# Optimization experiments

Measured on AMD Instinct MI355X. Metric: run time of the kernel, lower is better.

## Reference

```python
import jax, jax.numpy as jnp
import numpy as np

B, D, C, K = 131072, 512, 5, 10  # batch, emb_dim, num_classes, k experts


def setup_inputs() -> dict:
    key = jax.random.key(0)
    k1, k2, k3, k4, k5 = jax.random.split(key, 5)
    s = 1.0 / np.sqrt(D)
    return {
        "emb": jax.random.normal(k1, (B, D), dtype=jnp.float32),
        "We": jax.random.normal(k2, (K, D, C), dtype=jnp.float32) * s,
        "be": jax.random.normal(k3, (K, C), dtype=jnp.float32) * s,
        "Wg": jax.random.normal(k4, (D, K), dtype=jnp.float32) * s,
        "bg": jax.random.normal(k5, (K,), dtype=jnp.float32) * s,
    }


def reference(emb, We, be, Wg, bg):
    # gate: softmax over experts, [B, K]
    g = jax.nn.softmax(emb @ Wg + bg, axis=1)
    # all experts as one batched GEMM: [B, K, C], then ReLU
    e = jax.nn.relu(jnp.einsum('bd,kdc->bkc', emb, We) + be[None, :, :])
    # gate-weighted sum over experts -> [B, C]
    return jnp.einsum('bkc,bk->bc', e, g)
```

## Files before the change

### kernel.cpp

```cpp
#include <hip/hip_runtime.h>
#include <hip/hip_bf16.h>
#include <math.h>

#define BATCH   131072
#define DIM     512
#define NCLS    5
#define NEXP    10
#define NW      60
#define NCOL    64
#define PACK_TPB 256
#define TPB     512
#define ROWS_PER_BLOCK 128
#define EPS_STRIDE 68

typedef short bf16x8 __attribute__((ext_vector_type(8)));
typedef float f32x4  __attribute__((ext_vector_type(4)));

__global__ void pack_w_kernel(const float* __restrict__ We,
                              const float* __restrict__ be,
                              const float* __restrict__ Wg,
                              const float* __restrict__ bg,
                              unsigned short* __restrict__ wfrag,
                              float* __restrict__ bpack) {
    int idx = blockIdx.x * PACK_TPB + threadIdx.x;
    int c    = idx >> 11;
    int t    = (idx >> 9) & 3;
    int lane = (idx >> 3) & 63;
    int j    = idx & 7;
    int d = c * 32 + (lane >> 4) * 8 + j;
    int n = t * 16 + (lane & 15);
    float v = 0.0f;
    if (n < NEXP) {
        v = Wg[d * NEXP + n];
    } else if (n < NW) {
        int k  = (n - NEXP) / NCLS;
        int cc = (n - NEXP) % NCLS;
        v = We[(k * DIM + d) * NCLS + cc];
    }
    wfrag[idx] = __builtin_bit_cast(unsigned short, __float2bfloat16(v));
    if (idx < NCOL) {
        float bv = 0.0f;
        if (idx < NEXP) bv = bg[idx];
        else if (idx < NW) {
            int k  = (idx - NEXP) / NCLS;
            int cc = (idx - NEXP) % NCLS;
            bv = be[k * NCLS + cc];
        }
        bpack[idx] = bv;
    }
}

__global__ __launch_bounds__(TPB) void moe_mfma_kernel(
        const float* __restrict__ emb,
        const float4* __restrict__ wfrag4,
        const float* __restrict__ bpack,
        float* __restrict__ out) {
    __shared__ float4 smem4[4096];

    const int tid = threadIdx.x;

    #pragma unroll
    for (int i = 0; i < 8; ++i)
        smem4[i * TPB + tid] = wfrag4[i * TPB + tid];
    __syncthreads();

    const int w = tid >> 6;
    const int L = tid & 63;
    const int r = L & 15;
    const int q = L >> 4;

    const size_t rowBase = (size_t)blockIdx.x * ROWS_PER_BLOCK + w * 16;
    const float* arow = emb + (rowBase + r) * DIM + q * 8;
    const bf16x8* bl = reinterpret_cast<const bf16x8*>(smem4);

    f32x4 acc0 = {0.f, 0.f, 0.f, 0.f};
    f32x4 acc1 = acc0, acc2 = acc0, acc3 = acc0;

    #pragma unroll 4
    for (int c = 0; c < DIM / 32; ++c) {
        const float4* a4 = reinterpret_cast<const float4*>(arow + (size_t)c * 32);
        float4 a0 = a4[0];
        float4 a1 = a4[1];
        bf16x8 b0 = bl[(c * 4 + 0) * 64 + L];
        bf16x8 b1 = bl[(c * 4 + 1) * 64 + L];
        bf16x8 b2 = bl[(c * 4 + 2) * 64 + L];
        bf16x8 b3 = bl[(c * 4 + 3) * 64 + L];
        float av[8] = {a0.x, a0.y, a0.z, a0.w, a1.x, a1.y, a1.z, a1.w};
        bf16x8 af;
        #pragma unroll
        for (int j = 0; j < 8; ++j)
            af[j] = (short)__builtin_bit_cast(unsigned short, __float2bfloat16(av[j]));
        acc0 = __builtin_amdgcn_mfma_f32_16x16x32_bf16(af, b0, acc0, 0, 0, 0);
        acc1 = __builtin_amdgcn_mfma_f32_16x16x32_bf16(af, b1, acc1, 0, 0, 0);
        acc2 = __builtin_amdgcn_mfma_f32_16x16x32_bf16(af, b2, acc2, 0, 0, 0);
        acc3 = __builtin_amdgcn_mfma_f32_16x16x32_bf16(af, b3, acc3, 0, 0, 0);
    }

    __syncthreads();
    float* eps = reinterpret_cast<float*>(smem4);
    #pragma unroll
    for (int i = 0; i < 4; ++i) {
        int rowl = w * 16 + q * 4 + i;
        eps[rowl * EPS_STRIDE +  0 + r] = acc0[i];
        eps[rowl * EPS_STRIDE + 16 + r] = acc1[i];
        eps[rowl * EPS_STRIDE + 32 + r] = acc2[i];
        eps[rowl * EPS_STRIDE + 48 + r] = acc3[i];
    }
    __syncthreads();

    if (tid < ROWS_PER_BLOCK) {
        const float* row = eps + tid * EPS_STRIDE;
        float g[NEXP];
        float m = -INFINITY;
        #pragma unroll
        for (int k = 0; k < NEXP; ++k) {
            g[k] = row[k] + bpack[k];
            m = fmaxf(m, g[k]);
        }
        float s = 0.0f;
        #pragma unroll
        for (int k = 0; k < NEXP; ++k) {
            g[k] = __expf(g[k] - m);
            s += g[k];
        }
        float inv = 1.0f / s;

        float o[NCLS] = {0.f, 0.f, 0.f, 0.f, 0.f};
        #pragma unroll
        for (int k = 0; k < NEXP; ++k) {
            float gk = g[k] * inv;
            #pragma unroll
            for (int cc = 0; cc < NCLS; ++cc) {
                int n = NEXP + k * NCLS + cc;
                float e = row[n] + bpack[n];
                e = fmaxf(e, 0.0f);
                o[cc] = fmaf(gk, e, o[cc]);
            }
        }
        size_t ob = ((size_t)blockIdx.x * ROWS_PER_BLOCK + tid) * NCLS;
        #pragma unroll
        for (int cc = 0; cc < NCLS; ++cc) out[ob + cc] = o[cc];
    }
}

extern "C" void kernel_launch(void* const* d_in, const int* in_sizes, int n_in,
                              void* d_out, int out_size, void* d_ws, size_t ws_size,
                              hipStream_t stream) {
    const float* emb = (const float*)d_in[0];
    const float* We  = (const float*)d_in[1];
    const float* be  = (const float*)d_in[2];
    const float* Wg  = (const float*)d_in[3];
    const float* bg  = (const float*)d_in[4];
    float* out = (float*)d_out;

    unsigned short* wfrag = (unsigned short*)d_ws;
    float* bpack = (float*)((char*)d_ws + 32768 * sizeof(unsigned short));

    pack_w_kernel<<<(16 * 4 * 64 * 8) / PACK_TPB, PACK_TPB, 0, stream>>>(
        We, be, Wg, bg, wfrag, bpack);
    moe_mfma_kernel<<<BATCH / ROWS_PER_BLOCK, TPB, 0, stream>>>(
        emb, (const float4*)wfrag, bpack, out);
}
```

Before: 362.3 us.

## Process two 16-row tiles per wave with software-prefetched A loads

Each wave now computes 32 rows, so every B fragment read from LDS feeds two MFMAs, and the block covers 256 rows. The next k-step's emb loads are issued before the current step's MFMAs to hide global latency. The epilogue stride shrinks to 61 and skips unused columns so 256 rows fit in LDS. In exchange, register pressure rises with eight accumulators and prefetch buffers, and the grid has half as many blocks.

```diff
diff --git a/kernel.cpp b/kernel.cpp
--- a/kernel.cpp
+++ b/kernel.cpp
@@ -10,8 +10,8 @@
 #define NCOL    64
 #define PACK_TPB 256
 #define TPB     512
-#define ROWS_PER_BLOCK 128
-#define EPS_STRIDE 68
+#define ROWS_PER_BLOCK 256
+#define EPS_STRIDE 61
 
 typedef short bf16x8 __attribute__((ext_vector_type(8)));
 typedef float f32x4  __attribute__((ext_vector_type(4)));
@@ -50,7 +50,34 @@
     }
 }
 
-__global__ __launch_bounds__(TPB) void moe_mfma_kernel(
+#define CVT8(DST, VA, VB) do {                                               \
+    float _v[8] = {(VA).x, (VA).y, (VA).z, (VA).w,                           \
+                   (VB).x, (VB).y, (VB).z, (VB).w};                          \
+    _Pragma("unroll")                                                        \
+    for (int _j = 0; _j < 8; ++_j)                                           \
+        (DST)[_j] = (short)__builtin_bit_cast(unsigned short,                \
+                         __float2bfloat16(_v[_j]));                          \
+} while (0)
+
+#define KSTEP(C, A0A, A0B, A1A, A1B) do {                                    \
+    bf16x8 _b0 = bl[((C) * 4 + 0) * 64 + L];                                 \
+    bf16x8 _b1 = bl[((C) * 4 + 1) * 64 + L];                                 \
+    bf16x8 _b2 = bl[((C) * 4 + 2) * 64 + L];                                 \
+    bf16x8 _b3 = bl[((C) * 4 + 3) * 64 + L];                                 \
+    bf16x8 _af0, _af1;                                                       \
+    CVT8(_af0, A0A, A0B);                                                    \
+    CVT8(_af1, A1A, A1B);                                                    \
+    acc0[0] = __builtin_amdgcn_mfma_f32_16x16x32_bf16(_af0, _b0, acc0[0], 0, 0, 0); \
+    acc1[0] = __builtin_amdgcn_mfma_f32_16x16x32_bf16(_af1, _b0, acc1[0], 0, 0, 0); \
+    acc0[1] = __builtin_amdgcn_mfma_f32_16x16x32_bf16(_af0, _b1, acc0[1], 0, 0, 0); \
+    acc1[1] = __builtin_amdgcn_mfma_f32_16x16x32_bf16(_af1, _b1, acc1[1], 0, 0, 0); \
+    acc0[2] = __builtin_amdgcn_mfma_f32_16x16x32_bf16(_af0, _b2, acc0[2], 0, 0, 0); \
+    acc1[2] = __builtin_amdgcn_mfma_f32_16x16x32_bf16(_af1, _b2, acc1[2], 0, 0, 0); \
+    acc0[3] = __builtin_amdgcn_mfma_f32_16x16x32_bf16(_af0, _b3, acc0[3], 0, 0, 0); \
+    acc1[3] = __builtin_amdgcn_mfma_f32_16x16x32_bf16(_af1, _b3, acc1[3], 0, 0, 0); \
+} while (0)
+
+__global__ __launch_bounds__(TPB, 4) void moe_mfma_kernel(
         const float* __restrict__ emb,
         const float4* __restrict__ wfrag4,
         const float* __restrict__ bpack,
@@ -58,53 +85,63 @@
     __shared__ float4 smem4[4096];
 
     const int tid = threadIdx.x;
+    const int w = tid >> 6;
+    const int L = tid & 63;
+    const int r = L & 15;
+    const int q = L >> 4;
+
+    const size_t rowBase = (size_t)blockIdx.x * ROWS_PER_BLOCK + w * 32;
+    const float* ap0 = emb + (rowBase + r) * DIM + q * 8;
+    const float* ap1 = ap0 + 16 * DIM;
+
+    float4 n0a = *reinterpret_cast<const float4*>(ap0);
+    float4 n0b = *reinterpret_cast<const float4*>(ap0 + 4);
+    float4 n1a = *reinterpret_cast<const float4*>(ap1);
+    float4 n1b = *reinterpret_cast<const float4*>(ap1 + 4);
 
     #pragma unroll
     for (int i = 0; i < 8; ++i)
         smem4[i * TPB + tid] = wfrag4[i * TPB + tid];
     __syncthreads();
 
-    const int w = tid >> 6;
-    const int L = tid & 63;
-    const int r = L & 15;
-    const int q = L >> 4;
-
-    const size_t rowBase = (size_t)blockIdx.x * ROWS_PER_BLOCK + w * 16;
-    const float* arow = emb + (rowBase + r) * DIM + q * 8;
     const bf16x8* bl = reinterpret_cast<const bf16x8*>(smem4);
 
-    f32x4 acc0 = {0.f, 0.f, 0.f, 0.f};
-    f32x4 acc1 = acc0, acc2 = acc0, acc3 = acc0;
-
-    #pragma unroll 4
-    for (int c = 0; c < DIM / 32; ++c) {
-        const float4* a4 = reinterpret_cast<const float4*>(arow + (size_t)c * 32);
-        float4 a0 = a4[0];
-        float4 a1 = a4[1];
-        bf16x8 b0 = bl[(c * 4 + 0) * 64 + L];
-        bf16x8 b1 = bl[(c * 4 + 1) * 64 + L];
-        bf16x8 b2 = bl[(c * 4 + 2) * 64 + L];
-        bf16x8 b3 = bl[(c * 4 + 3) * 64 + L];
-        float av[8] = {a0.x, a0.y, a0.z, a0.w, a1.x, a1.y, a1.z, a1.w};
-        bf16x8 af;
-        #pragma unroll
-        for (int j = 0; j < 8; ++j)
-            af[j] = (short)__builtin_bit_cast(unsigned short, __float2bfloat16(av[j]));
-        acc0 = __builtin_amdgcn_mfma_f32_16x16x32_bf16(af, b0, acc0, 0, 0, 0);
-        acc1 = __builtin_amdgcn_mfma_f32_16x16x32_bf16(af, b1, acc1, 0, 0, 0);
-        acc2 = __builtin_amdgcn_mfma_f32_16x16x32_bf16(af, b2, acc2, 0, 0, 0);
-        acc3 = __builtin_amdgcn_mfma_f32_16x16x32_bf16(af, b3, acc3, 0, 0, 0);
-    }
+    f32x4 acc0[4] = {{0.f,0.f,0.f,0.f},{0.f,0.f,0.f,0.f},
+                     {0.f,0.f,0.f,0.f},{0.f,0.f,0.f,0.f}};
+    f32x4 acc1[4] = {{0.f,0.f,0.f,0.f},{0.f,0.f,0.f,0.f},
+                     {0.f,0.f,0.f,0.f},{0.f,0.f,0.f,0.f}};
+
+    #pragma unroll 5
+    for (int c = 0; c < DIM / 32 - 1; ++c) {
+        float4 a0a = n0a, a0b = n0b, a1a = n1a, a1b = n1b;
+        const float* p0 = ap0 + (c + 1) * 32;
+        const float* p1 = ap1 + (c + 1) * 32;
+        n0a = *reinterpret_cast<const float4*>(p0);
+        n0b = *reinterpret_cast<const float4*>(p0 + 4);
+        n1a = *reinterpret_cast<const float4*>(p1);
+        n1b = *reinterpret_cast<const float4*>(p1 + 4);
+        KSTEP(c, a0a, a0b, a1a, a1b);
+    }
+    KSTEP(DIM / 32 - 1, n0a, n0b, n1a, n1b);
 
     __syncthreads();
     float* eps = reinterpret_cast<float*>(smem4);
     #pragma unroll
     for (int i = 0; i < 4; ++i) {
-        int rowl = w * 16 + q * 4 + i;
-        eps[rowl * EPS_STRIDE +  0 + r] = acc0[i];
-        eps[rowl * EPS_STRIDE + 16 + r] = acc1[i];
-        eps[rowl * EPS_STRIDE + 32 + r] = acc2[i];
-        eps[rowl * EPS_STRIDE + 48 + r] = acc3[i];
+        int rl0 = w * 32 + q * 4 + i;
+        float* e0 = eps + rl0 * EPS_STRIDE + r;
+        e0[ 0] = acc0[0][i];
+        e0[16] = acc0[1][i];
+        e0[32] = acc0[2][i];
+        int rl1 = rl0 + 16;
+        float* e1 = eps + rl1 * EPS_STRIDE + r;
+        e1[ 0] = acc1[0][i];
+        e1[16] = acc1[1][i];
+        e1[32] = acc1[2][i];
+        if (r < 12) {
+            e0[48] = acc0[3][i];
+            e1[48] = acc1[3][i];
+        }
     }
     __syncthreads();
 
```

Result: slower. 370.9 us (+2.4%).
